# Performance work log

Hardware: AMD Instinct MI355X
Metric: run time of the kernel (lower is better)

## Reference

```python
import jax, jax.numpy as jnp
import numpy as np

# ---- Cl(3,0,1) algebra constants (generators e1,e2,e3 square to +1, e0 to 0) ----
def _cayley_cl301():
    metric = [1.0, 1.0, 1.0, 0.0]
    C = np.zeros((16, 16, 16), np.float32)
    for a in range(16):
        for b in range(16):
            s = 1.0
            for i in range(4):
                if (b >> i) & 1:
                    if bin(a >> (i + 1)).count('1') % 2:
                        s = -s
            for i in range(4):
                if ((a & b) >> i) & 1:
                    s *= metric[i]
            if s != 0.0:
                C[a, b, a ^ b] = s
    return C

_CAYLEY = _cayley_cl301()
_REV = np.array([(-1.0) ** (bin(i).count('1') * (bin(i).count('1') - 1) // 2) for i in range(16)], np.float32)
_GRADE_MAP = np.zeros(16, np.int32)  # matches _GRADE_MAP_16 (all zeros) in the source

def _gp(x, y):
    # geometric product: [B,16] x [B,16] -> [B,16]
    return jnp.einsum('bi,bj,ijk->bk', x, y, jnp.asarray(_CAYLEY))

def _normalize_rotor(R):
    R_rev = R * jnp.asarray(_REV)
    sq = jnp.clip(jnp.abs(_gp(R, R_rev)[..., 0:1]), 1e-6, None)
    return R / jnp.sqrt(sq)


def setup_inputs() -> dict:
    key = jax.random.key(0)
    ks = jax.random.split(key, 20)
    B, N, D, K, H, hd = 8, 2048, 16, 8, 4, 8
    f = lambda i, shape, s: jax.random.normal(ks[i], shape, jnp.float32) * s
    return {
        'state': f(0, (B, N, D), 1.0),
        'hypotheses': f(1, (B, K, 4), 1.0),
        'R_accum': f(2, (B, D), 1.0),
        'mask': jnp.ones((B, N), bool),
        'Wq': f(3, (D, H * hd), 0.25), 'bq': jnp.zeros((H * hd,), jnp.float32),
        'Wk': f(4, (D, H * hd), 0.25), 'bk': jnp.zeros((H * hd,), jnp.float32),
        'v_gains': jnp.ones((5,), jnp.float32),
        'W_act': f(5, (K, D, D), 0.25), 'b_act': jnp.zeros((K, D), jnp.float32),
        'W_hyp': f(6, (4, D), 0.25), 'b_hyp': jnp.zeros((D,), jnp.float32),
        'W_ws': f(7, (D, 4), 0.25), 'b_ws': jnp.zeros((4,), jnp.float32),
        'W_s1': f(8, (10, 64), 0.3), 'b_s1': jnp.zeros((64,), jnp.float32),
        'W_s2': f(9, (64, 5), 0.1), 'b_s2': jnp.zeros((5,), jnp.float32),
        'W_lift': f(10, (4, D), 0.25), 'b_lift': jnp.zeros((D,), jnp.float32),
        'Wg1': f(11, (2 * D, 64), 0.2), 'bg1': jnp.zeros((64,), jnp.float32),
        'Wg2': f(12, (64, D), 0.1), 'bg2': jnp.full((D,), -3.0, jnp.float32),  # gate bias init -3
        'Wc1': f(13, (2, 16), 0.3), 'bc1': jnp.zeros((16,), jnp.float32),
        'Wc2': f(14, (16, 1), 0.2), 'bc2': jnp.full((1,), -3.0, jnp.float32),
        'norm_scale': jnp.ones((D,), jnp.float32),
        'rotors': f(15, (K, D), 0.25),
    }


def reference(state, hypotheses, R_accum, mask, Wq, bq, Wk, bk, v_gains,
              W_act, b_act, W_hyp, b_hyp, W_ws, b_ws, W_s1, b_s1, W_s2, b_s2,
              W_lift, b_lift, Wg1, bg1, Wg2, bg2, Wc1, bc1, Wc2, bc2,
              norm_scale, rotors):
    B, N, D = state.shape
    K = hypotheses.shape[1]
    H, hd = 4, 8
    scale = hd ** -0.5

    # ---- CellAttention ----
    Q = (state @ Wq + bq).reshape(B, N, H, hd)
    Kt = (state @ Wk + bk).reshape(B, N, H, hd)
    scores = jnp.einsum('bnhd,bmhd->bhnm', Q, Kt) * scale
    scores = jnp.where(mask[:, None, None, :], scores, -jnp.inf)
    attn = jax.nn.softmax(scores, axis=-1)
    attn_avg = attn.mean(axis=1)                       # [B,N,N]
    attended = jnp.einsum('bnm,bmd->bnd', attn_avg, state)
    attended = attended * v_gains[jnp.asarray(_GRADE_MAP)]  # per-grade gains (grade_map all 0)

    # ---- masked world summary ----
    mask_f = mask.astype(state.dtype)[..., None]       # [B,N,1]
    cnt = jnp.clip(mask_f.sum(axis=1), 1.0, None)      # [B,1]
    world_summary = (attended * mask_f).sum(axis=1) / cnt  # [B,D]

    # ---- action proposals: K candidate states [B,K,N,D] ----
    hyp_feat = hypotheses @ W_hyp + b_hyp              # [B,K,D]
    candidates = jnp.tanh(jnp.einsum('bnd,kde->bkne', attended, W_act)
                          + b_act[None, :, None, :] + hyp_feat[:, :, None, :])

    # ---- FIM proxy: masked mean energy per hypothesis [B,K] ----
    fim = (jnp.square(candidates).mean(axis=-1) * mask_f[:, None, :, 0]).sum(axis=-1) / cnt

    # ---- search plane: evolve hypotheses + selection weights ----
    ws4 = world_summary @ W_ws + b_ws                  # [B,4]
    feat = jnp.concatenate([hypotheses,
                            jnp.broadcast_to(ws4[:, None, :], (B, K, 4)),
                            fim[..., None], fim[..., None]], axis=-1)  # [B,K,10]
    h = jax.nn.relu(feat @ W_s1 + b_s1)
    sp_out = h @ W_s2 + b_s2                           # [B,K,5]
    new_hyp = hypotheses + sp_out[..., :4]
    weights = jax.nn.softmax(sp_out[..., 4], axis=-1)  # [B,K]

    # ---- weighted candidate selection + grade-wise modulation ----
    new_state = jnp.einsum('bk,bknd->bnd', weights, candidates)
    agg = jnp.einsum('bk,bkc->bc', weights, new_hyp)   # [B,4]
    modulation = 1.0 + jnp.tanh(agg @ W_lift + b_lift) # [B,D]
    new_state = new_state * modulation[:, None, :]

    # ---- gated residual update ----
    gate_in = jnp.concatenate([state, new_state], axis=-1)     # [B,N,2D]
    gate = jax.nn.sigmoid(jax.nn.relu(gate_in @ Wg1 + bg1) @ Wg2 + bg2)  # [B,N,D]
    cg_in = jnp.stack([state[..., 0], new_state[..., 0]], axis=-1)       # [B,N,2]
    color_gate = jax.nn.sigmoid(jax.nn.relu(cg_in @ Wc1 + bc1) @ Wc2 + bc2)  # [B,N,1]
    spatial = gate[..., 1:] * new_state[..., 1:] + (1.0 - gate[..., 1:]) * state[..., 1:]
    color = color_gate * new_state[..., 0:1] + (1.0 - color_gate) * state[..., 0:1]
    ns = jnp.concatenate([color, spatial], axis=-1)

    # ---- Clifford layer norm (RMS over the 16 components, learnable scale) ----
    ns = ns * norm_scale / jnp.sqrt(jnp.mean(jnp.square(ns), axis=-1, keepdims=True) + 1e-6)

    # ---- rotor accumulation ----
    R_t = jnp.einsum('bk,kd->bd', weights, rotors)
    R_new = _normalize_rotor(_gp(R_t, jax.lax.stop_gradient(R_accum)))

    return ns, new_hyp, R_new, fim, weights, gate
```

## Files before the change

### kernel.cpp

```cpp
#include <hip/hip_runtime.h>
#include <hip/hip_bf16.h>
#include <math.h>

#define BB 8
#define NN 2048

#define WS_SUM  0
#define WS_FIM  128
#define WS_HF   192
#define WS_W    1216
#define WS_MOD  1280

#define OUT_NS   0
#define OUT_NH   (BB*NN*16)
#define OUT_RN   (OUT_NH + 256)
#define OUT_FIM  (OUT_RN + 128)
#define OUT_W    (OUT_FIM + 64)
#define OUT_GATE (OUT_W + 64)

typedef const float* fp;

__device__ __forceinline__ float fast_tanh(float x){
  float ax = fabsf(x);
  float u = __expf(-2.f*ax);
  float t = (1.f-u)/(1.f+u);
  return x < 0.f ? -t : t;
}
__device__ __forceinline__ float sigm(float x){ return 1.f/(1.f+__expf(-x)); }
__device__ __forceinline__ float cl_sign(int a, int b){
  int s = 1;
  #pragma unroll
  for(int i=0;i<4;i++) if((b>>i)&1){ if(__popc(a>>(i+1))&1) s = -s; }
  if(a & b & 8) return 0.f;
  return (float)s;
}
__device__ __forceinline__ float cl_rev(int a){
  int k = __popc(a);
  return ((k*(k-1)/2)&1) ? -1.f : 1.f;
}

__global__ void zero_kernel(float* __restrict__ ws){
  ws[WS_SUM + threadIdx.x] = 0.f;
}

__global__ __launch_bounds__(256) void flash_kernel(fp state, fp Wq, fp bq, fp Wk, fp bk,
                                                    fp vgains, float* __restrict__ ws,
                                                    float* __restrict__ out){
  __shared__ float wqs[512], wks[512], bqs[32], bks[32], sumbuf[16];
  __shared__ float ksh[128*36];
  __shared__ float ssh[128*20];
  int tid = threadIdx.x;
  int b = blockIdx.x >> 6;
  int tile = blockIdx.x & 63;
  int r = tid >> 3, s = tid & 7;
  int n = tile*32 + r;
  for(int l=tid; l<512; l+=256){ wqs[l]=Wq[l]; wks[l]=Wk[l]; }
  if(tid < 32){ bqs[tid]=bq[tid]; bks[tid]=bk[tid]; }
  if(tid < 16) sumbuf[tid]=0.f;
  __syncthreads();
  float q[32];
  { float st[16];
    const float4* sp = (const float4*)(state + (size_t)(b*NN+n)*16);
    #pragma unroll
    for(int i=0;i<4;i++){ float4 v=sp[i];
      st[4*i]=v.x; st[4*i+1]=v.y; st[4*i+2]=v.z; st[4*i+3]=v.w; }
    for(int c=0;c<32;c++){
      float a = bqs[c];
      #pragma unroll
      for(int d=0;d<16;d++) a += st[d]*wqs[d*32+c];
      q[c] = a;
    } }
  float l[4] = {0.f,0.f,0.f,0.f};
  float acc[4][16];
  #pragma unroll
  for(int h=0;h<4;h++)
    #pragma unroll
    for(int d=0;d<16;d++) acc[h][d]=0.f;
  const float scale = 0.35355339059327373f;
  const float* sb = state + (size_t)b*NN*16;
  for(int m0=0; m0<NN; m0+=128){
    __syncthreads();
    #pragma unroll
    for(int i=0;i<2;i++){
      int f = tid + i*256;
      int rw = f >> 2, c4 = f & 3;
      float4 v = ((const float4*)(sb + (size_t)(m0+rw)*16))[c4];
      *((float4*)(ssh + rw*20 + c4*4)) = v;
    }
    __syncthreads();
    {
      int rw = tid >> 1, c0 = (tid & 1)*16;
      float sr[16];
      #pragma unroll
      for(int d=0;d<16;d++) sr[d] = ssh[rw*20 + d];
      for(int cc=0;cc<16;cc++){
        int c = c0 + cc;
        float a = bks[c];
        #pragma unroll
        for(int d=0;d<16;d++) a += sr[d]*wks[d*32+c];
        ksh[rw*36 + c] = a;
      } }
    __syncthreads();
    for(int j=0;j<16;j++){
      int ml = (j<<3) + s;
      float kk[32], vv[16];
      { const float4* kp = (const float4*)(ksh + ml*36);
        #pragma unroll
        for(int i=0;i<8;i++){ float4 v=kp[i];
          kk[4*i]=v.x; kk[4*i+1]=v.y; kk[4*i+2]=v.z; kk[4*i+3]=v.w; }
        const float4* vp = (const float4*)(ssh + ml*20);
        #pragma unroll
        for(int i=0;i<4;i++){ float4 v=vp[i];
          vv[4*i]=v.x; vv[4*i+1]=v.y; vv[4*i+2]=v.z; vv[4*i+3]=v.w; } }
      #pragma unroll
      for(int h=0;h<4;h++){
        float sc = 0.f;
        #pragma unroll
        for(int i=0;i<8;i++) sc += q[h*8+i]*kk[h*8+i];
        float p = __expf(sc*scale);
        l[h] += p;
        #pragma unroll
        for(int d=0;d<16;d++) acc[h][d] += p*vv[d];
      }
    }
  }
  #pragma unroll
  for(int mask=1; mask<8; mask<<=1){
    #pragma unroll
    for(int h=0;h<4;h++){
      l[h] += __shfl_xor(l[h], mask);
      #pragma unroll
      for(int d=0;d<16;d++) acc[h][d] += __shfl_xor(acc[h][d], mask);
    }
  }
  if(s == 0){
    float gain = vgains[0] * 0.25f;
    float il[4];
    #pragma unroll
    for(int h=0;h<4;h++) il[h] = 1.f/l[h];
    float* ao = out + OUT_GATE + (size_t)(b*NN+n)*16;
    #pragma unroll
    for(int d=0;d<16;d++){
      float a = (acc[0][d]*il[0] + acc[1][d]*il[1] + acc[2][d]*il[2] + acc[3][d]*il[3]) * gain;
      ao[d] = a;
      atomicAdd(&sumbuf[d], a);
    }
  }
  __syncthreads();
  if(tid < 16) atomicAdd(ws + WS_SUM + b*16 + tid, sumbuf[tid]);
}

__global__ __launch_bounds__(256) void fim_kernel(fp hyp, fp W_act, fp b_act, fp W_hyp, fp b_hyp,
                                                  float* __restrict__ ws, float* __restrict__ out){
  __shared__ float wact[256], hf[16], ba[16], red[4];
  int tid = threadIdx.x;
  int b = blockIdx.x >> 3, k = blockIdx.x & 7;
  wact[tid] = W_act[k*256 + tid];
  if(tid < 16){
    float h = b_hyp[tid];
    #pragma unroll
    for(int c=0;c<4;c++) h += hyp[(b*8+k)*4+c] * W_hyp[c*16+tid];
    hf[tid] = h;
    ws[WS_HF + (b*8+k)*16 + tid] = h;
    ba[tid] = b_act[k*16+tid];
  }
  __syncthreads();
  const float* ag = out + OUT_GATE;
  float local = 0.f;
  for(int i=0;i<8;i++){
    int n = i*256 + tid;
    const float4* ap = (const float4*)(ag + (size_t)(b*NN+n)*16);
    float a[16];
    #pragma unroll
    for(int ii=0;ii<4;ii++){ float4 v=ap[ii];
      a[4*ii]=v.x; a[4*ii+1]=v.y; a[4*ii+2]=v.z; a[4*ii+3]=v.w; }
    #pragma unroll
    for(int e=0;e<16;e++){
      float t = ba[e] + hf[e];
      #pragma unroll
      for(int d=0;d<16;d++) t += a[d]*wact[d*16+e];
      float c = fast_tanh(t);
      local += c*c;
    }
  }
  #pragma unroll
  for(int m=32;m>=1;m>>=1) local += __shfl_xor(local, m);
  if((tid & 63) == 0) red[tid>>6] = local;
  __syncthreads();
  if(tid == 0){
    float f = (red[0]+red[1]+red[2]+red[3]) * (1.f/(16.f*2048.f));
    ws[WS_FIM + b*8 + k] = f;
    out[OUT_FIM + b*8 + k] = f;
  }
}

__global__ void head_kernel(fp hyp, fp racc, fp W_ws, fp b_ws, fp W_s1, fp b_s1,
                            fp W_s2, fp b_s2, fp W_lift, fp b_lift, fp rotors,
                            float* __restrict__ ws, float* __restrict__ out){
  int b = blockIdx.x, t = threadIdx.x;
  __shared__ float ws16[16], ws4v[4], hl[64], sp[8][5], w[8], nh[8][4], agg4[4], rt[16], rg[16], invn;
  if(t<16) ws16[t] = ws[WS_SUM + b*16 + t] * (1.f/2048.f);
  __syncthreads();
  if(t<4){
    float a = b_ws[t];
    for(int d=0;d<16;d++) a += ws16[d]*W_ws[d*4+t];
    ws4v[t] = a;
  }
  __syncthreads();
  for(int k=0;k<8;k++){
    float f[10];
    #pragma unroll
    for(int c=0;c<4;c++){ f[c] = hyp[(b*8+k)*4+c]; f[4+c] = ws4v[c]; }
    f[8] = f[9] = ws[WS_FIM + b*8 + k];
    float h = b_s1[t];
    #pragma unroll
    for(int i=0;i<10;i++) h += f[i]*W_s1[i*64+t];
    hl[t] = fmaxf(h, 0.f);
    __syncthreads();
    if(t<5){
      float a = b_s2[t];
      for(int j=0;j<64;j++) a += hl[j]*W_s2[j*5+t];
      sp[k][t] = a;
    }
    __syncthreads();
  }
  if(t<32){ int k=t>>2, c=t&3;
    float v = hyp[(b*8+k)*4+c] + sp[k][c];
    nh[k][c]=v; out[OUT_NH+(b*8+k)*4+c] = v; }
  if(t==0){
    float mx=-1e30f;
    for(int k=0;k<8;k++) mx = fmaxf(mx, sp[k][4]);
    float sm=0.f;
    for(int k=0;k<8;k++){ float e=__expf(sp[k][4]-mx); w[k]=e; sm+=e; }
    for(int k=0;k<8;k++) w[k] /= sm;
  }
  __syncthreads();
  if(t<8){ out[OUT_W+b*8+t]=w[t]; ws[WS_W+b*8+t]=w[t]; }
  if(t<4){ float a=0.f; for(int k=0;k<8;k++) a += w[k]*nh[k][t]; agg4[t]=a; }
  __syncthreads();
  if(t<16){
    float m = b_lift[t];
    for(int c=0;c<4;c++) m += agg4[c]*W_lift[c*16+t];
    ws[WS_MOD+b*16+t] = 1.f + fast_tanh(m);
    float rv=0.f;
    for(int k=0;k<8;k++) rv += w[k]*rotors[k*16+t];
    rt[t]=rv;
  }
  __syncthreads();
  if(t<16){
    float g=0.f;
    for(int a=0;a<16;a++) g += cl_sign(a, a^t)*rt[a]*racc[b*16+(a^t)];
    rg[t]=g;
  }
  __syncthreads();
  if(t==0){
    float sq=0.f;
    for(int a=0;a<16;a++) sq += cl_sign(a,a)*cl_rev(a)*rg[a]*rg[a];
    sq = fmaxf(fabsf(sq), 1e-6f);
    invn = 1.f/sqrtf(sq);
  }
  __syncthreads();
  if(t<16) out[OUT_RN+b*16+t] = rg[t]*invn;
}

__global__ __launch_bounds__(256) void final_kernel(fp state, fp W_act, fp b_act, fp Wg1, fp bg1,
    fp Wg2, fp bg2, fp Wc1, fp bc1, fp Wc2, fp bc2, fp norm_scale,
    float* __restrict__ ws, float* out){
  __shared__ float wact[2048];
  __shared__ float wg1[2048];
  __shared__ float wg2[1024];
  __shared__ float wc1s[32], wc2s[16], bc1s[16], bg1s[64], bg2s[16], bas[128], hfs[128], wts[8], mods[16], nscs[16];
  __shared__ float bc2s;
  int tid = threadIdx.x;
  int b = blockIdx.x >> 3;
  int n = (blockIdx.x & 7)*256 + tid;
  for(int i=tid;i<2048;i+=256){ wact[i]=W_act[i]; wg1[i]=Wg1[i]; }
  for(int i=tid;i<1024;i+=256) wg2[i]=Wg2[i];
  if(tid<64) bg1s[tid]=bg1[tid];
  if(tid<32) wc1s[tid]=Wc1[tid];
  if(tid<16){ wc2s[tid]=Wc2[tid]; bc1s[tid]=bc1[tid]; bg2s[tid]=bg2[tid];
              mods[tid]=ws[WS_MOD+b*16+tid]; nscs[tid]=norm_scale[tid]; }
  if(tid<128){ bas[tid]=b_act[tid]; hfs[tid]=ws[WS_HF+b*128+tid]; }
  if(tid<8) wts[tid]=ws[WS_W+b*8+tid];
  if(tid==0) bc2s=bc2[0];
  __syncthreads();
  float a[16], st[16];
  { const float4* ap=(const float4*)(out + OUT_GATE + (size_t)(b*NN+n)*16);
    #pragma unroll
    for(int i=0;i<4;i++){ float4 v=ap[i];
      a[4*i]=v.x; a[4*i+1]=v.y; a[4*i+2]=v.z; a[4*i+3]=v.w; }
    const float4* sp=(const float4*)(state+(size_t)(b*NN+n)*16);
    #pragma unroll
    for(int i=0;i<4;i++){ float4 u=sp[i];
      st[4*i]=u.x; st[4*i+1]=u.y; st[4*i+2]=u.z; st[4*i+3]=u.w; } }
  float nsv[16];
  #pragma unroll
  for(int e=0;e<16;e++) nsv[e]=0.f;
  for(int k=0;k<8;k++){
    float wk = wts[k];
    #pragma unroll
    for(int e=0;e<16;e++){
      float t = bas[k*16+e] + hfs[k*16+e];
      #pragma unroll
      for(int d=0;d<16;d++) t += a[d]*wact[k*256 + d*16 + e];
      nsv[e] += wk*fast_tanh(t);
    }
  }
  #pragma unroll
  for(int e=0;e<16;e++) nsv[e] *= mods[e];
  float gacc[16];
  #pragma unroll
  for(int e=0;e<16;e++) gacc[e]=bg2s[e];
  for(int j=0;j<64;j++){
    float h = bg1s[j];
    #pragma unroll
    for(int i=0;i<16;i++) h += st[i]*wg1[i*64+j];
    #pragma unroll
    for(int i=0;i<16;i++) h += nsv[i]*wg1[(16+i)*64+j];
    h = fmaxf(h, 0.f);
    #pragma unroll
    for(int e=0;e<16;e++) gacc[e] += h*wg2[j*16+e];
  }
  float gate[16];
  #pragma unroll
  for(int e=0;e<16;e++) gate[e]=sigm(gacc[e]);
  float cga = bc2s;
  for(int j=0;j<16;j++){
    float h = fmaxf(bc1s[j] + st[0]*wc1s[j] + nsv[0]*wc1s[16+j], 0.f);
    cga += h*wc2s[j];
  }
  float cg = sigm(cga);
  float nsx[16];
  nsx[0] = cg*nsv[0] + (1.f-cg)*st[0];
  #pragma unroll
  for(int e=1;e<16;e++) nsx[e] = gate[e]*nsv[e] + (1.f-gate[e])*st[e];
  float ms=0.f;
  #pragma unroll
  for(int e=0;e<16;e++) ms += nsx[e]*nsx[e];
  float rr = 1.f/sqrtf(ms*(1.f/16.f) + 1e-6f);
  float* po = out + (size_t)(b*NN+n)*16;
  float* pg = out + OUT_GATE + (size_t)(b*NN+n)*16;
  float nso[16], go[16];
  #pragma unroll
  for(int e=0;e<16;e++){ nso[e]=nsx[e]*nscs[e]*rr; go[e]=gate[e]; }
  #pragma unroll
  for(int i=0;i<4;i++){
    ((float4*)po)[i] = make_float4(nso[4*i], nso[4*i+1], nso[4*i+2], nso[4*i+3]);
    ((float4*)pg)[i] = make_float4(go[4*i], go[4*i+1], go[4*i+2], go[4*i+3]);
  }
}

extern "C" void kernel_launch(void* const* d_in, const int* in_sizes, int n_in,
                              void* d_out, int out_size, void* d_ws, size_t ws_size,
                              hipStream_t stream){
  (void)in_sizes; (void)n_in; (void)out_size; (void)ws_size;
  fp state = (fp)d_in[0];
  fp hyp   = (fp)d_in[1];
  fp racc  = (fp)d_in[2];
  fp Wq=(fp)d_in[4];  fp bq=(fp)d_in[5];
  fp Wk=(fp)d_in[6];  fp bk=(fp)d_in[7];
  fp vg=(fp)d_in[8];
  fp W_act=(fp)d_in[9];  fp b_act=(fp)d_in[10];
  fp W_hyp=(fp)d_in[11]; fp b_hyp=(fp)d_in[12];
  fp W_ws=(fp)d_in[13];  fp b_ws=(fp)d_in[14];
  fp W_s1=(fp)d_in[15];  fp b_s1=(fp)d_in[16];
  fp W_s2=(fp)d_in[17];  fp b_s2=(fp)d_in[18];
  fp W_lift=(fp)d_in[19]; fp b_lift=(fp)d_in[20];
  fp Wg1=(fp)d_in[21];   fp bg1=(fp)d_in[22];
  fp Wg2=(fp)d_in[23];   fp bg2=(fp)d_in[24];
  fp Wc1=(fp)d_in[25];   fp bc1=(fp)d_in[26];
  fp Wc2=(fp)d_in[27];   fp bc2=(fp)d_in[28];
  fp nsc=(fp)d_in[29];   fp rot=(fp)d_in[30];
  float* out = (float*)d_out;
  float* ws = (float*)d_ws;

  hipLaunchKernelGGL(zero_kernel,  dim3(1),   dim3(128), 0, stream, ws);
  hipLaunchKernelGGL(flash_kernel, dim3(512), dim3(256), 0, stream, state, Wq, bq, Wk, bk, vg, ws, out);
  hipLaunchKernelGGL(fim_kernel,   dim3(64),  dim3(256), 0, stream, hyp, W_act, b_act, W_hyp, b_hyp, ws, out);
  hipLaunchKernelGGL(head_kernel,  dim3(8),   dim3(64),  0, stream, hyp, racc, W_ws, b_ws, W_s1, b_s1,
                     W_s2, b_s2, W_lift, b_lift, rot, ws, out);
  hipLaunchKernelGGL(final_kernel, dim3(64),  dim3(256), 0, stream, state, W_act, b_act, Wg1, bg1,
                     Wg2, bg2, Wc1, bc1, Wc2, bc2, nsc, ws, out);
}
```

Before: 317.6 us.

## Precompute Q/K in separate kernel and widen grids of flash, fim, final

```diff
diff --git a/kernel.cpp b/kernel.cpp
--- a/kernel.cpp
+++ b/kernel.cpp
@@ -5,11 +5,13 @@
 #define BB 8
 #define NN 2048
 
-#define WS_SUM  0
-#define WS_FIM  128
-#define WS_HF   192
-#define WS_W    1216
-#define WS_MOD  1280
+#define WS_Q    0
+#define WS_K    (WS_Q + BB*NN*32)
+#define WS_SUM  (WS_K + BB*NN*32)
+#define WS_FIM  (WS_SUM + 128)
+#define WS_HF   (WS_FIM + 64)
+#define WS_W    (WS_HF + 1024)
+#define WS_MOD  (WS_W + 64)
 
 #define OUT_NS   0
 #define OUT_NH   (BB*NN*16)
@@ -43,33 +45,45 @@
   ws[WS_SUM + threadIdx.x] = 0.f;
 }
 
-__global__ __launch_bounds__(256) void flash_kernel(fp state, fp Wq, fp bq, fp Wk, fp bk,
-                                                    fp vgains, float* __restrict__ ws,
+__global__ __launch_bounds__(256) void qk_kernel(fp state, fp Wq, fp bq, fp Wk, fp bk,
+                                                 float* __restrict__ ws){
+  __shared__ float wq[512], wk[512], bqs[32], bks[32];
+  int tid = threadIdx.x;
+  for(int l = tid; l < 512; l += 256){ wq[l] = Wq[l]; wk[l] = Wk[l]; }
+  if(tid < 32){ bqs[tid] = bq[tid]; bks[tid] = bk[tid]; }
+  __syncthreads();
+  int row = blockIdx.x*256 + tid;
+  float s[16];
+  const float4* sp = (const float4*)(state + (size_t)row*16);
+  #pragma unroll
+  for(int i=0;i<4;i++){ float4 u = sp[i];
+    s[4*i]=u.x; s[4*i+1]=u.y; s[4*i+2]=u.z; s[4*i+3]=u.w; }
+  float* qo = ws + WS_Q + (size_t)row*32;
+  float* ko = ws + WS_K + (size_t)row*32;
+  for(int c=0;c<32;c++){
+    float qa = bqs[c], ka = bks[c];
+    #pragma unroll
+    for(int d=0;d<16;d++){ qa += s[d]*wq[d*32+c]; ka += s[d]*wk[d*32+c]; }
+    qo[c] = qa; ko[c] = ka;
+  }
+}
+
+__global__ __launch_bounds__(256) void flash_kernel(fp state, fp vgains, float* __restrict__ ws,
                                                     float* __restrict__ out){
-  __shared__ float wqs[512], wks[512], bqs[32], bks[32], sumbuf[16];
   __shared__ float ksh[128*36];
   __shared__ float ssh[128*20];
+  __shared__ float sumbuf[16];
   int tid = threadIdx.x;
-  int b = blockIdx.x >> 6;
-  int tile = blockIdx.x & 63;
-  int r = tid >> 3, s = tid & 7;
-  int n = tile*32 + r;
-  for(int l=tid; l<512; l+=256){ wqs[l]=Wq[l]; wks[l]=Wk[l]; }
-  if(tid < 32){ bqs[tid]=bq[tid]; bks[tid]=bk[tid]; }
-  if(tid < 16) sumbuf[tid]=0.f;
-  __syncthreads();
+  int b = blockIdx.x >> 7;
+  int tile = blockIdx.x & 127;
+  int r = tid >> 4, s = tid & 15;
+  int n = tile*16 + r;
+  if(tid < 16) sumbuf[tid] = 0.f;
   float q[32];
-  { float st[16];
-    const float4* sp = (const float4*)(state + (size_t)(b*NN+n)*16);
-    #pragma unroll
-    for(int i=0;i<4;i++){ float4 v=sp[i];
-      st[4*i]=v.x; st[4*i+1]=v.y; st[4*i+2]=v.z; st[4*i+3]=v.w; }
-    for(int c=0;c<32;c++){
-      float a = bqs[c];
-      #pragma unroll
-      for(int d=0;d<16;d++) a += st[d]*wqs[d*32+c];
-      q[c] = a;
-    } }
+  { const float4* qp = (const float4*)(ws + WS_Q + (size_t)(b*NN + n)*32);
+    #pragma unroll
+    for(int i=0;i<8;i++){ float4 v = qp[i];
+      q[4*i]=v.x; q[4*i+1]=v.y; q[4*i+2]=v.z; q[4*i+3]=v.w; } }
   float l[4] = {0.f,0.f,0.f,0.f};
   float acc[4][16];
   #pragma unroll
@@ -77,9 +91,17 @@
     #pragma unroll
     for(int d=0;d<16;d++) acc[h][d]=0.f;
   const float scale = 0.35355339059327373f;
+  const float* kb = ws + WS_K + (size_t)b*NN*32;
   const float* sb = state + (size_t)b*NN*16;
   for(int m0=0; m0<NN; m0+=128){
     __syncthreads();
+    #pragma unroll
+    for(int i=0;i<4;i++){
+      int f = tid + i*256;
+      int rw = f >> 3, c4 = f & 7;
+      float4 v = ((const float4*)(kb + (size_t)(m0+rw)*32))[c4];
+      *((float4*)(ksh + rw*36 + c4*4)) = v;
+    }
     #pragma unroll
     for(int i=0;i<2;i++){
       int f = tid + i*256;
@@ -88,21 +110,8 @@
       *((float4*)(ssh + rw*20 + c4*4)) = v;
     }
     __syncthreads();
-    {
-      int rw = tid >> 1, c0 = (tid & 1)*16;
-      float sr[16];
-      #pragma unroll
-      for(int d=0;d<16;d++) sr[d] = ssh[rw*20 + d];
-      for(int cc=0;cc<16;cc++){
-        int c = c0 + cc;
-        float a = bks[c];
-        #pragma unroll
-        for(int d=0;d<16;d++) a += sr[d]*wks[d*32+c];
-        ksh[rw*36 + c] = a;
-      } }
-    __syncthreads();
-    for(int j=0;j<16;j++){
-      int ml = (j<<3) + s;
+    for(int j=0;j<8;j++){
+      int ml = (j<<4) + s;
       float kk[32], vv[16];
       { const float4* kp = (const float4*)(ksh + ml*36);
         #pragma unroll
@@ -125,7 +134,7 @@
     }
   }
   #pragma unroll
-  for(int mask=1; mask<8; mask<<=1){
+  for(int mask=1; mask<16; mask<<=1){
     #pragma unroll
     for(int h=0;h<4;h++){
       l[h] += __shfl_xor(l[h], mask);
@@ -138,7 +147,7 @@
     float il[4];
     #pragma unroll
     for(int h=0;h<4;h++) il[h] = 1.f/l[h];
-    float* ao = out + OUT_GATE + (size_t)(b*NN+n)*16;
+    float* ao = out + OUT_GATE + (size_t)(b*NN + n)*16;
     #pragma unroll
     for(int d=0;d<16;d++){
       float a = (acc[0][d]*il[0] + acc[1][d]*il[1] + acc[2][d]*il[2] + acc[3][d]*il[3]) * gain;
@@ -154,21 +163,21 @@
                                                   float* __restrict__ ws, float* __restrict__ out){
   __shared__ float wact[256], hf[16], ba[16], red[4];
   int tid = threadIdx.x;
-  int b = blockIdx.x >> 3, k = blockIdx.x & 7;
+  int b = blockIdx.x >> 5, k = (blockIdx.x >> 2) & 7, seg = blockIdx.x & 3;
   wact[tid] = W_act[k*256 + tid];
   if(tid < 16){
     float h = b_hyp[tid];
     #pragma unroll
     for(int c=0;c<4;c++) h += hyp[(b*8+k)*4+c] * W_hyp[c*16+tid];
     hf[tid] = h;
-    ws[WS_HF + (b*8+k)*16 + tid] = h;
+    if(seg == 0) ws[WS_HF + (b*8+k)*16 + tid] = h;
     ba[tid] = b_act[k*16+tid];
   }
   __syncthreads();
   const float* ag = out + OUT_GATE;
   float local = 0.f;
-  for(int i=0;i<8;i++){
-    int n = i*256 + tid;
+  for(int i=0;i<2;i++){
+    int n = seg*512 + i*256 + tid;
     const float4* ap = (const float4*)(ag + (size_t)(b*NN+n)*16);
     float a[16];
     #pragma unroll
@@ -187,11 +196,8 @@
   for(int m=32;m>=1;m>>=1) local += __shfl_xor(local, m);
   if((tid & 63) == 0) red[tid>>6] = local;
   __syncthreads();
-  if(tid == 0){
-    float f = (red[0]+red[1]+red[2]+red[3]) * (1.f/(16.f*2048.f));
-    ws[WS_FIM + b*8 + k] = f;
-    out[OUT_FIM + b*8 + k] = f;
-  }
+  if(tid == 0)
+    atomicAdd(ws + WS_FIM + b*8 + k, red[0]+red[1]+red[2]+red[3]);
 }
 
 __global__ void head_kernel(fp hyp, fp racc, fp W_ws, fp b_ws, fp W_s1, fp b_s1,
@@ -199,7 +205,12 @@
                             float* __restrict__ ws, float* __restrict__ out){
   int b = blockIdx.x, t = threadIdx.x;
   __shared__ float ws16[16], ws4v[4], hl[64], sp[8][5], w[8], nh[8][4], agg4[4], rt[16], rg[16], invn;
+  __shared__ float s1[640], s2[320], fims[8];
+  for(int i=t;i<640;i+=64) s1[i]=W_s1[i];
+  for(int i=t;i<320;i+=64) s2[i]=W_s2[i];
   if(t<16) ws16[t] = ws[WS_SUM + b*16 + t] * (1.f/2048.f);
+  if(t<8){ float f = ws[WS_FIM + b*8 + t] * (1.f/(16.f*2048.f));
+           fims[t]=f; out[OUT_FIM + b*8 + t] = f; }
   __syncthreads();
   if(t<4){
     float a = b_ws[t];
@@ -211,15 +222,15 @@
     float f[10];
     #pragma unroll
     for(int c=0;c<4;c++){ f[c] = hyp[(b*8+k)*4+c]; f[4+c] = ws4v[c]; }
-    f[8] = f[9] = ws[WS_FIM + b*8 + k];
+    f[8] = f[9] = fims[k];
     float h = b_s1[t];
     #pragma unroll
-    for(int i=0;i<10;i++) h += f[i]*W_s1[i*64+t];
+    for(int i=0;i<10;i++) h += f[i]*s1[i*64+t];
     hl[t] = fmaxf(h, 0.f);
     __syncthreads();
     if(t<5){
       float a = b_s2[t];
-      for(int j=0;j<64;j++) a += hl[j]*W_s2[j*5+t];
+      for(int j=0;j<64;j++) a += hl[j]*s2[j*5+t];
       sp[k][t] = a;
     }
     __syncthreads();
@@ -263,7 +274,7 @@
   if(t<16) out[OUT_RN+b*16+t] = rg[t]*invn;
 }
 
-__global__ __launch_bounds__(256) void final_kernel(fp state, fp W_act, fp b_act, fp Wg1, fp bg1,
+__global__ __launch_bounds__(64) void final_kernel(fp state, fp W_act, fp b_act, fp Wg1, fp bg1,
     fp Wg2, fp bg2, fp Wc1, fp bc1, fp Wc2, fp bc2, fp norm_scale,
     float* __restrict__ ws, float* out){
   __shared__ float wact[2048];
@@ -272,15 +283,16 @@
   __shared__ float wc1s[32], wc2s[16], bc1s[16], bg1s[64], bg2s[16], bas[128], hfs[128], wts[8], mods[16], nscs[16];
   __shared__ float bc2s;
   int tid = threadIdx.x;
-  int b = blockIdx.x >> 3;
-  int n = (blockIdx.x & 7)*256 + tid;
-  for(int i=tid;i<2048;i+=256){ wact[i]=W_act[i]; wg1[i]=Wg1[i]; }
-  for(int i=tid;i<1024;i+=256) wg2[i]=Wg2[i];
+  int b = blockIdx.x >> 5;
+  int n = (blockIdx.x & 31)*64 + tid;
+  for(int i=tid;i<2048;i+=64){ wact[i]=W_act[i]; wg1[i]=Wg1[i]; }
+  for(int i=tid;i<1024;i+=64) wg2[i]=Wg2[i];
   if(tid<64) bg1s[tid]=bg1[tid];
   if(tid<32) wc1s[tid]=Wc1[tid];
   if(tid<16){ wc2s[tid]=Wc2[tid]; bc1s[tid]=bc1[tid]; bg2s[tid]=bg2[tid];
               mods[tid]=ws[WS_MOD+b*16+tid]; nscs[tid]=norm_scale[tid]; }
-  if(tid<128){ bas[tid]=b_act[tid]; hfs[tid]=ws[WS_HF+b*128+tid]; }
+  if(tid>=32 && tid<32+16){ int i=tid-32; (void)i; }
+  for(int i=tid;i<128;i+=64){ bas[i]=b_act[i]; hfs[i]=ws[WS_HF+b*128+i]; }
   if(tid<8) wts[tid]=ws[WS_W+b*8+tid];
   if(tid==0) bc2s=bc2[0];
   __syncthreads();
@@ -374,11 +386,12 @@
   float* out = (float*)d_out;
   float* ws = (float*)d_ws;
 
-  hipLaunchKernelGGL(zero_kernel,  dim3(1),   dim3(128), 0, stream, ws);
-  hipLaunchKernelGGL(flash_kernel, dim3(512), dim3(256), 0, stream, state, Wq, bq, Wk, bk, vg, ws, out);
-  hipLaunchKernelGGL(fim_kernel,   dim3(64),  dim3(256), 0, stream, hyp, W_act, b_act, W_hyp, b_hyp, ws, out);
-  hipLaunchKernelGGL(head_kernel,  dim3(8),   dim3(64),  0, stream, hyp, racc, W_ws, b_ws, W_s1, b_s1,
+  hipLaunchKernelGGL(zero_kernel,  dim3(1),    dim3(192), 0, stream, ws);
+  hipLaunchKernelGGL(qk_kernel,    dim3(64),   dim3(256), 0, stream, state, Wq, bq, Wk, bk, ws);
+  hipLaunchKernelGGL(flash_kernel, dim3(1024), dim3(256), 0, stream, state, vg, ws, out);
+  hipLaunchKernelGGL(fim_kernel,   dim3(256),  dim3(256), 0, stream, hyp, W_act, b_act, W_hyp, b_hyp, ws, out);
+  hipLaunchKernelGGL(head_kernel,  dim3(8),    dim3(64),  0, stream, hyp, racc, W_ws, b_ws, W_s1, b_s1,
                      W_s2, b_s2, W_lift, b_lift, rot, ws, out);
-  hipLaunchKernelGGL(final_kernel, dim3(64),  dim3(256), 0, stream, state, W_act, b_act, Wg1, bg1,
+  hipLaunchKernelGGL(final_kernel, dim3(256),  dim3(64),  0, stream, state, W_act, b_act, Wg1, bg1,
                      Wg2, bg2, Wc1, bc1, Wc2, bc2, nsc, ws, out);
 }
```

New measurement: 518.2 us. 63.2% more time.
